# Kernel tuning notes

Measured on AMD Instinct MI355X. Metric: run time of the kernel, lower is better.

The kernel has to match this reference:

```python
import jax, jax.numpy as jnp
import numpy as np

B, L, D, H, KV = 2, 2048, 2048, 16, 4
K = D // H  # head dim = 128
ROPE_BASE = 10000.0


def _rope_tables(seq_len, dim):
    inv_freq = 1.0 / (ROPE_BASE ** (jnp.arange(0, dim, 2, dtype=jnp.float32) / dim))
    t = jnp.arange(seq_len, dtype=jnp.float32)
    freqs = jnp.outer(t, inv_freq)  # [L, dim/2]
    return jnp.cos(freqs), jnp.sin(freqs)


def _apply_rope(x, cos, sin):
    # x: [B, h, L, K]; interleaved-pair rotation, matching torch stack+flatten
    x1 = x[..., ::2]
    x2 = x[..., 1::2]
    c = cos[None, None, :, :]
    s = sin[None, None, :, :]
    o1 = x1 * c - x2 * s
    o2 = x1 * s + x2 * c
    return jnp.stack((o1, o2), axis=-1).reshape(x.shape)


def setup_inputs() -> dict:
    key = jax.random.key(0)
    ks = jax.random.split(key, 5)
    scale = D ** -0.5
    return {
        "x": jax.random.normal(ks[0], (B, L, D), jnp.float32),
        "wq": jax.random.normal(ks[1], (D, D), jnp.float32) * scale,
        "wk": jax.random.normal(ks[2], (KV * K, D), jnp.float32) * scale,
        "wv": jax.random.normal(ks[3], (KV * K, D), jnp.float32) * scale,
        "wo": jax.random.normal(ks[4], (D, D), jnp.float32) * scale,
    }


def reference(x, wq, wk, wv, wo):
    Bx, Lx, Dx = x.shape
    # projections (nn.Linear: y = x @ W.T)
    q = (x @ wq.T).reshape(Bx, Lx, H, K).transpose(0, 2, 1, 3)   # [B,H,L,K]
    k = (x @ wk.T).reshape(Bx, Lx, KV, K).transpose(0, 2, 1, 3)  # [B,KV,L,K]
    v = (x @ wv.T).reshape(Bx, Lx, KV, K).transpose(0, 2, 1, 3)
    cos, sin = _rope_tables(Lx, K)
    q = _apply_rope(q, cos, sin)
    k = _apply_rope(k, cos, sin)
    # GQA: repeat_interleave KV heads to H heads
    rep = H // KV
    k = jnp.repeat(k, rep, axis=1)
    v = jnp.repeat(v, rep, axis=1)
    scores = jnp.einsum('bhqd,bhkd->bhqk', q, k) / jnp.sqrt(jnp.float32(K))
    causal = jnp.tril(jnp.ones((Lx, Lx), dtype=bool))
    scores = jnp.where(causal[None, None], scores, jnp.finfo(scores.dtype).min)
    attn = jax.nn.softmax(scores, axis=-1)
    out = jnp.einsum('bhqk,bhkd->bhqd', attn, v)
    out = out.transpose(0, 2, 1, 3).reshape(Bx, Lx, Dx)
    return out @ wo.T
```

## Files before the change

kernel.cpp:

```cpp
#include <hip/hip_runtime.h>
#include <stdint.h>

#define DEV static __device__ __forceinline__

typedef __attribute__((ext_vector_type(8))) short s16x8;
typedef __attribute__((ext_vector_type(4))) short s16x4;
typedef __attribute__((ext_vector_type(4))) float f32x4;

constexpr int BB = 2, LL = 2048, DD = 2048, NH = 16, NKV = 4, HD = 128;
constexpr int Mrows = BB * LL;
constexpr int NQKV = DD + 2 * NKV * HD;

DEV ushort f2bf(float f){
  union { float f; uint32_t u; } v; v.f = f;
  uint32_t u = v.u;
  u += 0x7fffu + ((u >> 16) & 1u);
  return (ushort)(u >> 16);
}
DEV float bf2f(ushort h){
  union { uint32_t u; float f; } v; v.u = ((uint32_t)h) << 16;
  return v.f;
}

DEV f32x4 mfma32(s16x8 a, s16x8 b, f32x4 c){
  return __builtin_amdgcn_mfma_f32_16x16x32_bf16(a, b, c, 0, 0, 0);
}
DEV f32x4 mfma16(s16x4 a, s16x4 b, f32x4 c){
#if __has_builtin(__builtin_amdgcn_mfma_f32_16x16x16bf16_1k)
  return __builtin_amdgcn_mfma_f32_16x16x16bf16_1k(a, b, c, 0, 0, 0);
#else
  asm volatile("v_mfma_f32_16x16x16_bf16 %0, %1, %2, %0" : "+v"(c) : "v"(a), "v"(b));
  return c;
#endif
}

DEV float vmax4(f32x4 v){ return fmaxf(fmaxf(v[0], v[1]), fmaxf(v[2], v[3])); }
DEV float vsum4(f32x4 v){ return (v[0] + v[1]) + (v[2] + v[3]); }

__global__ void cvt_all_kernel(const float* __restrict__ x, const float* __restrict__ wq,
                               const float* __restrict__ wk, const float* __restrict__ wv,
                               const float* __restrict__ wo,
                               ushort* __restrict__ xb, ushort* __restrict__ wqkv,
                               ushort* __restrict__ wob){
  constexpr int C0 = Mrows * DD / 4;
  constexpr int C1 = C0 + DD * DD / 4;
  constexpr int C2 = C1 + NKV * HD * DD / 4;
  constexpr int C3 = C2 + NKV * HD * DD / 4;
  constexpr int C4 = C3 + DD * DD / 4;
  int stride = gridDim.x * blockDim.x;
  for (int i = blockIdx.x * blockDim.x + threadIdx.x; i < C4; i += stride){
    const float* src; ushort* dst; int j;
    if (i < C0){ src = x;  dst = xb;                              j = i; }
    else if (i < C1){ src = wq; dst = wqkv;                       j = i - C0; }
    else if (i < C2){ src = wk; dst = wqkv + (size_t)DD * DD;     j = i - C1; }
    else if (i < C3){ src = wv; dst = wqkv + (size_t)(DD + NKV*HD) * DD; j = i - C2; }
    else { src = wo; dst = wob;                                   j = i - C3; }
    float4 v = reinterpret_cast<const float4*>(src)[j];
    ushort4 o = make_ushort4(f2bf(v.x), f2bf(v.y), f2bf(v.z), f2bf(v.w));
    reinterpret_cast<ushort4*>(dst)[j] = o;
  }
}

__global__ void rope_table_kernel(float* __restrict__ cosT, float* __restrict__ sinT){
  int i = blockIdx.x * blockDim.x + threadIdx.x;
  if (i >= LL * 64) return;
  int l = i >> 6, f = i & 63;
  float inv = __expf(-logf(10000.f) * (float)f / 64.f);
  float ang = (float)l * inv;
  float s, c;
  sincosf(ang, &s, &c);
  cosT[i] = c; sinT[i] = s;
}

__global__ void rope_qk_kernel(ushort* __restrict__ q, ushort* __restrict__ k,
                               const float* __restrict__ cosT, const float* __restrict__ sinT){
  constexpr int TQ = BB * NH * LL * 16;
  constexpr int TK = BB * NKV * LL * 16;
  int idx = blockIdx.x * blockDim.x + threadIdx.x;
  if (idx >= TQ + TK) return;
  ushort* t; float scale; int id;
  if (idx < TQ){ t = q; id = idx; scale = 0.08838834764831845f; }
  else { t = k; id = idx - TQ; scale = 1.0f; }
  int c = id & 15;
  int l = (id >> 4) & (LL - 1);
  s16x8 v = *reinterpret_cast<const s16x8*>(t + (size_t)id * 8);
  int fb = (l << 6) + c * 4;
  s16x8 o;
  #pragma unroll
  for (int j = 0; j < 4; ++j){
    float x1 = bf2f((ushort)v[2*j]);
    float x2 = bf2f((ushort)v[2*j+1]);
    float co = cosT[fb + j], si = sinT[fb + j];
    o[2*j]   = (short)f2bf((x1 * co - x2 * si) * scale);
    o[2*j+1] = (short)f2bf((x1 * si + x2 * co) * scale);
  }
  *reinterpret_cast<s16x8*>(t + (size_t)id * 8) = o;
}

DEV void g2l16(const void* g, void* l){
  __builtin_amdgcn_global_load_lds((__attribute__((address_space(1))) void*)(void*)g,
                                   (__attribute__((address_space(3))) void*)l, 16, 0, 0);
}

#define GPHASE(DB, KK, MH, SDB, SKH, SB, ST, VM) { \
    const ushort* As_ = Asm + ((DB)*2 + (KK)) * 8192 + wm * 128 * 32; \
    const ushort* Bs_ = Bsm + ((DB)*2 + (KK)) * 8192 + wn * 64 * 32; \
    s16x8 af_[4], bf_[4]; \
    _Pragma("unroll") \
    for (int i_ = 0; i_ < 4; ++i_) \
      af_[i_] = *(const s16x8*)&As_[(((MH)*4 + i_) * 16 + lr) * 32 + swz]; \
    _Pragma("unroll") \
    for (int n_ = 0; n_ < 4; ++n_) \
      bf_[n_] = *(const s16x8*)&Bs_[(n_ * 16 + lr) * 32 + swz]; \
    STG(SDB, SKH, SB, ST); \
    if (VM) asm volatile("s_waitcnt vmcnt(4)" ::: "memory"); \
    __builtin_amdgcn_s_barrier(); \
    __builtin_amdgcn_s_setprio(1); \
    _Pragma("unroll") \
    for (int i_ = 0; i_ < 4; ++i_) \
      _Pragma("unroll") \
      for (int n_ = 0; n_ < 4; ++n_) \
        acc[(MH)*4 + i_][n_] = mfma32(af_[i_], bf_[n_], acc[(MH)*4 + i_][n_]); \
    __builtin_amdgcn_s_setprio(0); \
    __builtin_amdgcn_s_barrier(); \
  }

template<int MODE>
__global__ __launch_bounds__(512, 2) void gemm256_kernel(const ushort* __restrict__ A,
    const ushort* __restrict__ W, float* __restrict__ fout, ushort* __restrict__ qo,
    ushort* __restrict__ ko, ushort* __restrict__ vo)
{
  extern __shared__ ushort smem[];
  ushort* Asm = smem;
  ushort* Bsm = smem + 32768;
  const int tid = threadIdx.x;
  const int w = tid >> 6, lane = tid & 63;
  const int lr = lane & 15, lg = lane >> 4;
  const int wm = w >> 2, wn = w & 3;
  const int swz = (lg ^ ((lr >> 1) & 3)) * 8;
  const int cpx = (int)gridDim.x >> 3;
  const int id = (int)blockIdx.x;
  const int nid = (id & 7) * cpx + (id >> 3);
  const int bx = nid >> 4, by = nid & 15;
  const int brow = by * 256, bcol = bx * 256;

  const int schunk = ((lane & 3) ^ ((lane >> 3) & 3)) * 8;
  const ushort* gA = A + (size_t)(brow + w*32 + (lane >> 2)) * 2048 + schunk;
  const ushort* gW = W + (size_t)(bcol + w*32 + (lane >> 2)) * 2048 + schunk;
  const int ldsOff = w * 1024 + lane * 8;

  f32x4 acc[8][4] = {};

  auto STG = [&](int db, int kh, int isB, int tile){
    const ushort* g = (isB ? gW : gA) + tile * 64 + kh * 32;
    ushort* l = (isB ? Bsm : Asm) + (db*2 + kh) * 8192 + ldsOff;
    g2l16(g, l);
    g2l16(g + 16 * 2048, l + 512);
  };

  STG(0,0,0,0); STG(0,0,1,0); STG(0,1,0,0); STG(0,1,1,0); STG(1,0,0,1); STG(1,0,1,1);
  asm volatile("s_waitcnt vmcnt(4)" ::: "memory");
  __builtin_amdgcn_s_barrier();

  for (int it = 0; it < 16; ++it){
    const int t  = 2 * it;
    const int t2 = (t + 2 < 32) ? t + 2 : 31;
    const int t3 = (t + 3 < 32) ? t + 3 : 31;
    GPHASE(0,0,0, 1,1,0, t+1, 0);
    GPHASE(0,0,1, 1,1,1, t+1, 0);
    GPHASE(0,1,0, 0,0,0, t2,  0);
    GPHASE(0,1,1, 0,0,1, t2,  1);
    GPHASE(1,0,0, 0,1,0, t2,  0);
    GPHASE(1,0,1, 0,1,1, t2,  0);
    GPHASE(1,1,0, 1,0,0, t3,  0);
    GPHASE(1,1,1, 1,0,1, t3,  1);
  }
  asm volatile("s_waitcnt vmcnt(0)" ::: "memory");

  #pragma unroll
  for (int mf = 0; mf < 8; ++mf)
    #pragma unroll
    for (int nf = 0; nf < 4; ++nf)
      #pragma unroll
      for (int r = 0; r < 4; ++r){
        int row = brow + wm*128 + mf*16 + lg*4 + r;
        int col = bcol + wn*64 + nf*16 + lr;
        float v = acc[mf][nf][r];
        if (MODE == 0){
          fout[(size_t)row * DD + col] = v;
        } else {
          int b = row >> 11, l = row & (LL - 1);
          ushort bv = f2bf(v);
          if (col < DD){
            qo[(((size_t)(b * NH + (col >> 7))) * LL + l) * HD + (col & 127)] = bv;
          } else if (col < DD + NKV * HD){
            int c = col - DD;
            ko[(((size_t)(b * NKV + (c >> 7))) * LL + l) * HD + (c & 127)] = bv;
          } else {
            int c = col - DD - NKV * HD;
            vo[(((size_t)(b * NKV + (c >> 7))) * HD + (c & 127)) * LL + l] = bv;
          }
        }
      }
}

template<int NQ>
DEV void tile_step(const ushort* __restrict__ Ks, const ushort* __restrict__ Vs,
                   const s16x8 (*qf)[4], f32x4 (*of)[8], float* mrun, float* lrun,
                   const int* qrow, int jb, int lr, int lg)
{
  f32x4 s[4][NQ];
  #pragma unroll
  for (int kt = 0; kt < 4; ++kt)
    #pragma unroll
    for (int q = 0; q < NQ; ++q) s[kt][q] = (f32x4){0.f, 0.f, 0.f, 0.f};

  __builtin_amdgcn_s_setprio(1);
  #pragma unroll
  for (int kk = 0; kk < 4; ++kk)
    #pragma unroll
    for (int kt = 0; kt < 4; ++kt){
      s16x8 kf = *reinterpret_cast<const s16x8*>(
          &Ks[((kt*16 + lr) << 7) + (((kk*4 + lg) ^ (lr & 7)) << 3)]);
      #pragma unroll
      for (int q = 0; q < NQ; ++q)
        s[kt][q] = mfma32(kf, qf[q][kk], s[kt][q]);
    }
  __builtin_amdgcn_s_setprio(0);

  #pragma unroll
  for (int q = 0; q < NQ; ++q)
    if (jb + 63 > qrow[q]){
      int qg = qrow[q] + lr;
      #pragma unroll
      for (int kt = 0; kt < 4; ++kt){
        int kvg = jb + kt*16 + lg*4;
        #pragma unroll
        for (int r = 0; r < 4; ++r)
          if (kvg + r > qg) s[kt][q][r] = -1e30f;
      }
    }

  float mx[NQ];
  #pragma unroll
  for (int q = 0; q < NQ; ++q){
    mx[q] = fmaxf(fmaxf(vmax4(s[0][q]), vmax4(s[1][q])),
                  fmaxf(vmax4(s[2][q]), vmax4(s[3][q])));
    mx[q] = fmaxf(mx[q], __shfl_xor(mx[q], 16, 64));
    mx[q] = fmaxf(mx[q], __shfl_xor(mx[q], 32, 64));
  }
  int small = 1;
  #pragma unroll
  for (int q = 0; q < NQ; ++q) small &= (mx[q] <= mrun[q] + 8.f);
  if (!__all(small)){
    #pragma unroll
    for (int q = 0; q < NQ; ++q){
      float mn = fmaxf(mrun[q], mx[q]);
      float fac = __expf(mrun[q] - mn);
      mrun[q] = mn;
      lrun[q] *= fac;
      #pragma unroll
      for (int f = 0; f < 8; ++f) of[q][f] *= fac;
    }
  }
  float ps[NQ];
  #pragma unroll
  for (int q = 0; q < NQ; ++q) ps[q] = 0.f;
  #pragma unroll
  for (int kt = 0; kt < 4; ++kt)
    #pragma unroll
    for (int q = 0; q < NQ; ++q){
      #pragma unroll
      for (int r = 0; r < 4; ++r)
        s[kt][q][r] = __expf(s[kt][q][r] - mrun[q]);
      ps[q] += vsum4(s[kt][q]);
    }
  #pragma unroll
  for (int q = 0; q < NQ; ++q){
    ps[q] += __shfl_xor(ps[q], 16, 64);
    ps[q] += __shfl_xor(ps[q], 32, 64);
    lrun[q] += ps[q];
  }
  s16x4 pb[4][NQ];
  #pragma unroll
  for (int kt = 0; kt < 4; ++kt)
    #pragma unroll
    for (int q = 0; q < NQ; ++q){
      s16x4 pv;
      #pragma unroll
      for (int r = 0; r < 4; ++r) pv[r] = (short)f2bf(s[kt][q][r]);
      pb[kt][q] = pv;
    }
  __builtin_amdgcn_s_setprio(1);
  #pragma unroll
  for (int f = 0; f < 8; ++f)
    #pragma unroll
    for (int kt = 0; kt < 4; ++kt){
      s16x4 va = *reinterpret_cast<const s16x4*>(
          &Vs[((f*16 + lr) << 6) + (((2*kt + (lg >> 1)) ^ (lr & 7)) << 3) + ((lg & 1) << 2)]);
      #pragma unroll
      for (int q = 0; q < NQ; ++q)
        of[q][f] = mfma16(va, pb[kt][q], of[q][f]);
    }
  __builtin_amdgcn_s_setprio(0);
}

__global__ __launch_bounds__(256) void attn_kernel(const ushort* __restrict__ Q,
    const ushort* __restrict__ Kg, const ushort* __restrict__ VTg, ushort* __restrict__ O)
{
  __shared__ ushort Ksm[2][64 * 128];
  __shared__ ushort Vsm[2][128 * 64];
  const int tid = threadIdx.x;
  const int w = tid >> 6, lane = tid & 63;
  const int lr = lane & 15, lg = lane >> 4;
  const int id = blockIdx.x;
  const int nid = (id & 7) * 64 + (id >> 3);
  const int pair = nid & 15;
  const int bh = nid >> 4;
  const int b = bh >> 4, h = bh & 15, kvh = h >> 2;
  const size_t qoff = (size_t)bh * LL * HD;
  const size_t koff = (size_t)(b * NKV + kvh) * LL * HD;
  const size_t voff = (size_t)(b * NKV + kvh) * HD * LL;
  const int qrow[2] = { pair*64 + w*16, (31 - pair)*64 + w*16 };
  const int nt  = 32 - pair;
  const int ntA = pair + 1;

  s16x8 qf[2][4];
  #pragma unroll
  for (int qt = 0; qt < 2; ++qt)
    #pragma unroll
    for (int kk = 0; kk < 4; ++kk)
      qf[qt][kk] = *reinterpret_cast<const s16x8*>(
          &Q[qoff + (size_t)(qrow[qt] + lr) * HD + kk*32 + lg*8]);

  f32x4 of[2][8] = {};
  float mrun[2] = {-1e30f, -1e30f}, lrun[2] = {0.f, 0.f};

  auto STAGE = [&](int buf, int jb){
    #pragma unroll
    for (int it = 0; it < 4; ++it){
      int chunk = it * 256 + tid;
      int r = chunk >> 4, c = chunk & 15;
      g2l16(Kg + koff + (size_t)(jb + r) * HD + ((c ^ (r & 7)) << 3), &Ksm[buf][chunk << 3]);
    }
    #pragma unroll
    for (int it = 0; it < 4; ++it){
      int chunk = it * 256 + tid;
      int r = chunk >> 3, c = chunk & 7;
      g2l16(VTg + voff + (size_t)r * LL + jb + ((c ^ (r & 7)) << 3), &Vsm[buf][chunk << 3]);
    }
  };
  STAGE(0, 0);

  for (int t = 0; t < nt; ++t){
    const int jb = t << 6, cur = t & 1;
    __syncthreads();
    if (t + 1 < nt) STAGE(cur ^ 1, (t + 1) << 6);
    if (t < ntA)
      tile_step<2>(Ksm[cur], Vsm[cur], qf, of, mrun, lrun, qrow, jb, lr, lg);
    else
      tile_step<1>(Ksm[cur], Vsm[cur], qf + 1, of + 1, mrun + 1, lrun + 1, qrow + 1, jb, lr, lg);
  }

  #pragma unroll
  for (int qt = 0; qt < 2; ++qt){
    float inv = 1.0f / lrun[qt];
    #pragma unroll
    for (int f = 0; f < 8; ++f)
      #pragma unroll
      for (int r = 0; r < 4; ++r){
        int row = qrow[qt] + lr;
        int col = h * HD + f*16 + lg*4 + r;
        O[((size_t)b * LL + row) * DD + col] = f2bf(of[qt][f][r] * inv);
      }
  }
}

extern "C" void kernel_launch(void* const* d_in, const int* in_sizes, int n_in,
                              void* d_out, int out_size, void* d_ws, size_t ws_size,
                              hipStream_t stream)
{
  const float* x  = (const float*)d_in[0];
  const float* wq = (const float*)d_in[1];
  const float* wk = (const float*)d_in[2];
  const float* wv = (const float*)d_in[3];
  const float* wo = (const float*)d_in[4];
  float* out = (float*)d_out;

  char* p = (char*)d_ws;
  auto alloc = [&](size_t bytes) -> void* {
    void* r = (void*)p; p += (bytes + 255) & ~(size_t)255; return r;
  };
  ushort* xb    = (ushort*)alloc((size_t)Mrows * DD * 2);
  ushort* wqkvb = (ushort*)alloc((size_t)NQKV * DD * 2);
  ushort* wob   = (ushort*)alloc((size_t)DD * DD * 2);
  ushort* qws   = (ushort*)alloc((size_t)BB * NH * LL * HD * 2);
  ushort* kws   = (ushort*)alloc((size_t)BB * NKV * LL * HD * 2);
  ushort* vws   = (ushort*)alloc((size_t)BB * NKV * LL * HD * 2);
  ushort* aows  = (ushort*)alloc((size_t)Mrows * DD * 2);
  float*  cosT  = (float*)alloc((size_t)LL * 64 * 4);
  float*  sinT  = (float*)alloc((size_t)LL * 64 * 4);

  hipFuncSetAttribute(reinterpret_cast<const void*>(gemm256_kernel<1>),
                      hipFuncAttributeMaxDynamicSharedMemorySize, 131072);
  hipFuncSetAttribute(reinterpret_cast<const void*>(gemm256_kernel<0>),
                      hipFuncAttributeMaxDynamicSharedMemorySize, 131072);

  hipLaunchKernelGGL(cvt_all_kernel, dim3(2048), dim3(256), 0, stream,
                     x, wq, wk, wv, wo, xb, wqkvb, wob);
  hipLaunchKernelGGL(rope_table_kernel, dim3((LL*64)/256), dim3(256), 0, stream, cosT, sinT);

  hipLaunchKernelGGL(gemm256_kernel<1>, dim3(192), dim3(512), 131072, stream,
                     xb, wqkvb, (float*)nullptr, qws, kws, vws);

  {
    constexpr int tot = BB*NH*LL*16 + BB*NKV*LL*16;
    hipLaunchKernelGGL(rope_qk_kernel, dim3(tot/256), dim3(256), 0, stream,
                       qws, kws, cosT, sinT);
  }

  hipLaunchKernelGGL(attn_kernel, dim3(512), dim3(256), 0, stream,
                     qws, kws, vws, aows);

  hipLaunchKernelGGL(gemm256_kernel<0>, dim3(128), dim3(512), 131072, stream,
                     aows, wob, out, (ushort*)nullptr, (ushort*)nullptr, (ushort*)nullptr);
}
```

Baseline: 375.0 us.

## Split-K the output projection GEMM and remap attention blocks across heads

The output projection GEMM is split along K into two halves launched as a 2D grid (256 blocks instead of 128), so it fills more of the CUs. Partial results are combined with float atomicAdd into an output buffer that is zeroed beforehand with a memset. The attention block mapping is also reordered so adjacent blocks interleave batches, heads and mirrored query pairs, to balance causal work across the dispatch order. The cost is atomic traffic on the output, an extra memset, and non-deterministic float summation order.

```diff
diff --git a/kernel.cpp b/kernel.cpp
--- a/kernel.cpp
+++ b/kernel.cpp
@@ -128,7 +128,7 @@
 template<int MODE>
 __global__ __launch_bounds__(512, 2) void gemm256_kernel(const ushort* __restrict__ A,
     const ushort* __restrict__ W, float* __restrict__ fout, ushort* __restrict__ qo,
-    ushort* __restrict__ ko, ushort* __restrict__ vo)
+    ushort* __restrict__ ko, ushort* __restrict__ vo, int ntiles)
 {
   extern __shared__ ushort smem[];
   ushort* Asm = smem;
@@ -143,10 +143,11 @@
   const int nid = (id & 7) * cpx + (id >> 3);
   const int bx = nid >> 4, by = nid & 15;
   const int brow = by * 256, bcol = bx * 256;
+  const int kbase = (int)blockIdx.y * ntiles * 64;
 
   const int schunk = ((lane & 3) ^ ((lane >> 3) & 3)) * 8;
-  const ushort* gA = A + (size_t)(brow + w*32 + (lane >> 2)) * 2048 + schunk;
-  const ushort* gW = W + (size_t)(bcol + w*32 + (lane >> 2)) * 2048 + schunk;
+  const ushort* gA = A + (size_t)(brow + w*32 + (lane >> 2)) * 2048 + kbase + schunk;
+  const ushort* gW = W + (size_t)(bcol + w*32 + (lane >> 2)) * 2048 + kbase + schunk;
   const int ldsOff = w * 1024 + lane * 8;
 
   f32x4 acc[8][4] = {};
@@ -162,10 +163,11 @@
   asm volatile("s_waitcnt vmcnt(4)" ::: "memory");
   __builtin_amdgcn_s_barrier();
 
-  for (int it = 0; it < 16; ++it){
+  const int tmax = ntiles - 1;
+  for (int it = 0; it < (ntiles >> 1); ++it){
     const int t  = 2 * it;
-    const int t2 = (t + 2 < 32) ? t + 2 : 31;
-    const int t3 = (t + 3 < 32) ? t + 3 : 31;
+    const int t2 = (t + 2 < tmax) ? t + 2 : tmax;
+    const int t3 = (t + 3 < tmax) ? t + 3 : tmax;
     GPHASE(0,0,0, 1,1,0, t+1, 0);
     GPHASE(0,0,1, 1,1,1, t+1, 0);
     GPHASE(0,1,0, 0,0,0, t2,  0);
@@ -187,7 +189,7 @@
         int col = bcol + wn*64 + nf*16 + lr;
         float v = acc[mf][nf][r];
         if (MODE == 0){
-          fout[(size_t)row * DD + col] = v;
+          atomicAdd(&fout[(size_t)row * DD + col], v);
         } else {
           int b = row >> 11, l = row & (LL - 1);
           ushort bv = f2bf(v);
@@ -315,8 +317,11 @@
   const int lr = lane & 15, lg = lane >> 4;
   const int id = blockIdx.x;
   const int nid = (id & 7) * 64 + (id >> 3);
-  const int pair = nid & 15;
-  const int bh = nid >> 4;
+  const int q4 = nid & 15;
+  const int b4 = (nid >> 4) & 1;
+  const int hi = (nid >> 5) & 1;
+  const int bh = (nid >> 6) * 4 + b4 * 2 + hi;
+  const int pair = hi ? (15 - q4) : q4;
   const int b = bh >> 4, h = bh & 15, kvh = h >> 2;
   const size_t qoff = (size_t)bh * LL * HD;
   const size_t koff = (size_t)(b * NKV + kvh) * LL * HD;
@@ -406,12 +411,14 @@
   hipFuncSetAttribute(reinterpret_cast<const void*>(gemm256_kernel<0>),
                       hipFuncAttributeMaxDynamicSharedMemorySize, 131072);
 
+  hipMemsetAsync(out, 0, (size_t)Mrows * DD * sizeof(float), stream);
+
   hipLaunchKernelGGL(cvt_all_kernel, dim3(2048), dim3(256), 0, stream,
                      x, wq, wk, wv, wo, xb, wqkvb, wob);
   hipLaunchKernelGGL(rope_table_kernel, dim3((LL*64)/256), dim3(256), 0, stream, cosT, sinT);
 
   hipLaunchKernelGGL(gemm256_kernel<1>, dim3(192), dim3(512), 131072, stream,
-                     xb, wqkvb, (float*)nullptr, qws, kws, vws);
+                     xb, wqkvb, (float*)nullptr, qws, kws, vws, 32);
 
   {
     constexpr int tot = BB*NH*LL*16 + BB*NKV*LL*16;
@@ -422,6 +429,6 @@
   hipLaunchKernelGGL(attn_kernel, dim3(512), dim3(256), 0, stream,
                      qws, kws, vws, aows);
 
-  hipLaunchKernelGGL(gemm256_kernel<0>, dim3(128), dim3(512), 131072, stream,
-                     aows, wob, out, (ushort*)nullptr, (ushort*)nullptr, (ushort*)nullptr);
-}
+  hipLaunchKernelGGL(gemm256_kernel<0>, dim3(128, 2), dim3(512), 131072, stream,
+                     aows, wob, out, (ushort*)nullptr, (ushort*)nullptr, (ushort*)nullptr, 16);
+}
```

Result: slower. 416.5 us (+11.1%).
